# Kernel optimization log

Measured on AMD Instinct MI355X. Metric: run time of the kernel, lower is better.

The kernel has to match this reference:

```python
import jax, jax.numpy as jnp
import numpy as np

NUM_HEADS = 12

def setup_inputs() -> dict:
    key = jax.random.key(0)
    ks = jax.random.split(key, 6)
    B, N, C = 16, 1024, 768
    H, d = NUM_HEADS, C // NUM_HEADS
    return {
        "x": jax.random.normal(ks[0], (B, N, C), dtype=jnp.float32),
        "W_qkv": jax.random.normal(ks[1], (C, 3 * C), dtype=jnp.float32) * 0.02,
        "b_qkv": jax.random.normal(ks[2], (3 * C,), dtype=jnp.float32) * 0.02,
        "zeta": jnp.ones((1, 1, H, 1, d), dtype=jnp.float32),
        "W_proj": jax.random.normal(ks[3], (C, C), dtype=jnp.float32) * 0.02,
        "b_proj": jax.random.normal(ks[4], (C,), dtype=jnp.float32) * 0.02,
        "mask": jnp.zeros((B, N), dtype=bool),
    }

def reference(x, W_qkv, b_qkv, zeta, W_proj, b_proj, mask):
    B, N, C = x.shape
    H = NUM_HEADS
    d = C // H
    scale = d ** -0.5
    # qkv: (B,N,3C) -> (B,N,3,H,d) -> (3,B,H,N,d), gated by zeta (1,1,H,1,d)
    qkv = (x @ W_qkv + b_qkv).reshape(B, N, 3, H, d).transpose(2, 0, 3, 1, 4)
    qkv = qkv * zeta
    q, k, v = qkv[0], qkv[1], qkv[2]
    attn = jnp.einsum("bhnd,bhmd->bhnm", q, k) * scale
    # mask (B,N) over keys -> (B,1,1,N)
    attn = jnp.where(mask[:, None, None, :], -jnp.inf, attn)
    attn = jax.nn.softmax(attn, axis=-1)
    out = jnp.einsum("bhnm,bhmd->bhnd", attn, v)          # (B,H,N,d)
    out = out.transpose(0, 2, 1, 3).reshape(B, N, C)
    return out @ W_proj + b_proj
```

## Files before the change

### kernel.cpp

```cpp
#include <hip/hip_runtime.h>
#include <hip/hip_bf16.h>

typedef unsigned short ushort_t;
typedef __bf16 bf16_t;
typedef bf16_t bf16x8 __attribute__((ext_vector_type(8)));
typedef float floatx4 __attribute__((ext_vector_type(4)));
typedef ushort_t ushortx8 __attribute__((ext_vector_type(8)));

struct alignas(8) us4 { ushort_t x, y, z, w; };

__device__ __forceinline__ ushort_t f2bf(float f) {
  union { float f; unsigned int u; } v; v.f = f;
  unsigned int u = v.u;
  return (ushort_t)((u + 0x7fffu + ((u >> 16) & 1u)) >> 16);
}

__device__ __forceinline__ unsigned int pk_bf16(float a, float b) {
  __hip_bfloat162 h = __float22bfloat162_rn(float2{a, b});
  union { __hip_bfloat162 h; unsigned int u; } v; v.h = h;
  return v.u;
}

__device__ __forceinline__ void async16(const void* g, void* l) {
  __builtin_amdgcn_global_load_lds(
      (const __attribute__((address_space(1))) unsigned int*)g,
      (__attribute__((address_space(3))) unsigned int*)l, 16, 0, 0);
}

#define LOG2E 1.44269504088896340736f


__global__ __launch_bounds__(256) void k_prep(const float* __restrict__ x,
                                              ushort_t* __restrict__ xb,
                                              const float* __restrict__ Wq,
                                              ushort_t* __restrict__ WqT,
                                              const float* __restrict__ Wp,
                                              ushort_t* __restrict__ WpT) {
  __shared__ float tile[32][33];
  const int bid = blockIdx.x, t = threadIdx.x;
  if (bid < 6144) {
    size_t i = ((size_t)bid * 256 + t) * 8;
    float4 a = *(const float4*)(x + i);
    float4 b = *(const float4*)(x + i + 4);
    ushortx8 o;
    o[0] = f2bf(a.x); o[1] = f2bf(a.y); o[2] = f2bf(a.z); o[3] = f2bf(a.w);
    o[4] = f2bf(b.x); o[5] = f2bf(b.y); o[6] = f2bf(b.z); o[7] = f2bf(b.w);
    *(ushortx8*)(xb + i) = o;
    return;
  }
  const float* in; ushort_t* out; int C, c0, r0;
  if (bid < 7872) {
    int b2 = bid - 6144;
    in = Wq; out = WqT; C = 2304;
    c0 = (b2 % 72) * 32; r0 = (b2 / 72) * 32;
  } else {
    int b3 = bid - 7872;
    in = Wp; out = WpT; C = 768;
    c0 = (b3 % 24) * 32; r0 = (b3 / 24) * 32;
  }
  const int tx = t & 31, ty = t >> 5;
#pragma unroll
  for (int i = 0; i < 32; i += 8)
    tile[ty + i][tx] = in[(size_t)(r0 + ty + i) * C + c0 + tx];
  __syncthreads();
#pragma unroll
  for (int i = 0; i < 32; i += 8)
    out[(size_t)(c0 + ty + i) * 768 + r0 + tx] = f2bf(tile[tx][ty + i]);
}


template <bool SWAP>
__device__ __forceinline__ void gemm_pipe3(const ushort_t* __restrict__ A,
                                           const ushort_t* __restrict__ Bt,
                                           int m0, int n0,
                                           ushort_t* sA, ushort_t* sB,
                                           floatx4 acc[4][4]) {
  const int t = threadIdx.x;
  const int lane = t & 63;
  const int lr = lane & 15, qd = lane >> 4;
  const int w = t >> 6;
  const int wr = w >> 1, wc = w & 1;
  const int swz = ((t & 3) ^ ((t >> 3) & 3)) * 8;
  const ushort_t* gA = A + (size_t)(m0 + (t >> 2)) * 768 + swz;
  const ushort_t* gB = Bt + (size_t)(n0 + (t >> 2)) * 768 + swz;
  char* lA = (char*)sA + t * 16;
  char* lB = (char*)sB + t * 16;
  const int rsz = (qd ^ ((lr >> 1) & 3)) * 16;
#define ISSUE(kk, buf)                                    \
  do {                                                    \
    const int k0_ = (kk) * 32, b_ = (buf) * 8192;         \
    async16(gA + k0_, lA + b_);                           \
    async16(gA + k0_ + 64 * 768, lA + b_ + 4096);         \
    async16(gB + k0_, lB + b_);                           \
    async16(gB + k0_ + 64 * 768, lB + b_ + 4096);         \
  } while (0)
  ISSUE(0, 0);
  ISSUE(1, 1);
  asm volatile("s_waitcnt vmcnt(4)" ::: "memory");
  asm volatile("s_barrier" ::: "memory");
#pragma unroll
  for (int k = 0; k < 24; ++k) {
    if (k + 2 < 24) ISSUE(k + 2, (k + 2) % 3);
    const char* cA = (const char*)sA + (k % 3) * 8192;
    const char* cB = (const char*)sB + (k % 3) * 8192;
    bf16x8 af[4], bfr[4];
#pragma unroll
    for (int i = 0; i < 4; ++i)
      af[i] = *(const bf16x8*)(cA + (wr * 64 + i * 16 + lr) * 64 + rsz);
#pragma unroll
    for (int j = 0; j < 4; ++j)
      bfr[j] = *(const bf16x8*)(cB + (wc * 64 + j * 16 + lr) * 64 + rsz);
#pragma unroll
    for (int i = 0; i < 4; ++i)
#pragma unroll
      for (int j = 0; j < 4; ++j) {
        if constexpr (SWAP)
          acc[i][j] = __builtin_amdgcn_mfma_f32_16x16x32_bf16(bfr[j], af[i], acc[i][j], 0, 0, 0);
        else
          acc[i][j] = __builtin_amdgcn_mfma_f32_16x16x32_bf16(af[i], bfr[j], acc[i][j], 0, 0, 0);
      }
    if (k < 22)
      asm volatile("s_waitcnt vmcnt(4)" ::: "memory");
    else if (k == 22)
      asm volatile("s_waitcnt vmcnt(0)" ::: "memory");
    if (k < 23) asm volatile("s_barrier" ::: "memory");
  }
#undef ISSUE
}


__global__ __launch_bounds__(256, 3) void k_qkv(const ushort_t* __restrict__ xb,
                                                const ushort_t* __restrict__ WqT,
                                                const float* __restrict__ bqkv,
                                                const float* __restrict__ zeta,
                                                ushort_t* __restrict__ qb,
                                                ushort_t* __restrict__ kb,
                                                ushort_t* __restrict__ vtb) {
  __shared__ alignas(16) ushort_t sA[3 * 4096];
  __shared__ alignas(16) ushort_t sB[3 * 4096];
  floatx4 acc[4][4] = {};
  const int lin = blockIdx.x;
  const int xcd = lin & 7, idx = lin >> 3;
  const int m0 = (xcd * 16 + (idx & 15)) * 128;
  const int n0 = (idx >> 4) * 128;
  const int tq = n0 / 768;
  const int t = threadIdx.x, lane = t & 63, w = t >> 6;
  const int wr = w >> 1, wc = w & 1, lr = lane & 15, qd = lane >> 4;
  if (tq < 2) {
    gemm_pipe3<true>(xb, WqT, m0, n0, sA, sB, acc);
    ushort_t* dst = (tq == 0) ? qb : kb;
    const float sc = (tq == 0) ? 0.125f * LOG2E : 1.0f;
#pragma unroll
    for (int j = 0; j < 4; ++j) {
      int n = n0 + wc * 64 + j * 16 + qd * 4;
      int nc = n - tq * 768;
      int h = nc >> 6, dim = n & 63;
      float4 b4 = *(const float4*)&bqkv[n];
      float4 z4 = *(const float4*)&zeta[nc];
      float g0 = z4.x * sc, g1 = z4.y * sc, g2 = z4.z * sc, g3 = z4.w * sc;
#pragma unroll
      for (int i = 0; i < 4; ++i) {
        int m = m0 + wr * 64 + i * 16 + lr;
        int b = m >> 10, seq = m & 1023;
        us4 pk;
        pk.x = f2bf((acc[i][j][0] + b4.x) * g0);
        pk.y = f2bf((acc[i][j][1] + b4.y) * g1);
        pk.z = f2bf((acc[i][j][2] + b4.z) * g2);
        pk.w = f2bf((acc[i][j][3] + b4.w) * g3);
        *(us4*)&dst[(((size_t)b * 12 + h) * 1024 + seq) * 64 + dim] = pk;
      }
    }
  } else {
    gemm_pipe3<false>(xb, WqT, m0, n0, sA, sB, acc);
#pragma unroll
    for (int j = 0; j < 4; ++j) {
      int n = n0 + wc * 64 + j * 16 + lr;
      int nc = n - 2 * 768;
      int h = nc >> 6, dim = n & 63;
      float bias = bqkv[n];
      float zv = zeta[nc];
#pragma unroll
      for (int i = 0; i < 4; ++i) {
        int mbase = m0 + wr * 64 + i * 16 + qd * 4;
        int b = mbase >> 10, seq = mbase & 1023;
        us4 pk;
        pk.x = f2bf((acc[i][j][0] + bias) * zv);
        pk.y = f2bf((acc[i][j][1] + bias) * zv);
        pk.z = f2bf((acc[i][j][2] + bias) * zv);
        pk.w = f2bf((acc[i][j][3] + bias) * zv);
        *(us4*)&vtb[(((size_t)b * 12 + h) * 64 + dim) * 1024 + seq] = pk;
      }
    }
  }
}


__global__ __launch_bounds__(256, 3) void k_attn(const ushort_t* __restrict__ qg,
                                                 const ushort_t* __restrict__ kg,
                                                 const ushort_t* __restrict__ vg,
                                                 const unsigned char* __restrict__ mask,
                                                 ushort_t* __restrict__ ob) {
  __shared__ alignas(16) char smem[49664];
  char* sV = smem + 32768;
  float* maskadd = (float*)(smem + 49152);
  const int t = threadIdx.x, lane = t & 63, w = t >> 6;
  const int lr = lane & 15, qd = lane >> 4;
  const int lin = blockIdx.x;
  const int bh = (lin & 7) + 8 * (lin >> 6);
  const int qt = (lin >> 3) & 7;
  const int b = bh / 12, h = bh % 12;
  const int qrow0 = qt * 128 + w * 32;
  const ushort_t* qp = qg + (size_t)bh * 65536;
  const ushort_t* kp = kg + (size_t)bh * 65536;
  const ushort_t* vp = vg + (size_t)bh * 65536;
  const unsigned char* mp = mask + b * 1024;

  bf16x8 qf[2][2];
#pragma unroll
  for (int ns = 0; ns < 2; ++ns)
#pragma unroll
    for (int kk = 0; kk < 2; ++kk)
      qf[ns][kk] = *(const bf16x8*)(qp + (size_t)(qrow0 + ns * 16 + lr) * 64 + kk * 32 + qd * 8);

  floatx4 o[4][2] = {};
  float lst[2] = {0.f, 0.f};
  char* sPw = smem + 16384 + w * 4096;

  for (int kt = 0; kt < 8; ++kt) {
    __syncthreads();
    const ushort_t* kpt = kp + kt * 8192;
#pragma unroll
    for (int it = 0; it < 4; ++it) {
      int p = it * 256 + t;
      int r = p >> 3, cs = (p & 7) ^ (r & 7);
      async16(kpt + r * 64 + cs * 8, smem + p * 16);
    }
    const ushort_t* vpt = vp + kt * 128;
#pragma unroll
    for (int it = 0; it < 4; ++it) {
      int p = it * 256 + t;
      int r = p >> 4, cs = (p & 15) ^ (r & 15);
      async16(vpt + (size_t)r * 1024 + cs * 8, sV + p * 16);
    }
    if (t < 128) maskadd[t] = mp[kt * 128 + t] ? -1e30f : 0.0f;
    asm volatile("s_waitcnt vmcnt(0)" ::: "memory");
    __syncthreads();

#pragma unroll
    for (int hh = 0; hh < 2; ++hh) {
      floatx4 s[4][2] = {};
#pragma unroll
      for (int kk = 0; kk < 2; ++kk) {
#pragma unroll
        for (int ms = 0; ms < 4; ++ms) {
          bf16x8 ak = *(const bf16x8*)(smem + ((hh * 4 + ms) * 16 + lr) * 128 +
                                       ((kk * 4 + qd) ^ (lr & 7)) * 16);
#pragma unroll
          for (int ns = 0; ns < 2; ++ns)
            s[ms][ns] = __builtin_amdgcn_mfma_f32_16x16x32_bf16(ak, qf[ns][kk], s[ms][ns], 0, 0, 0);
        }
      }
#pragma unroll
      for (int ms = 0; ms < 4; ++ms) {
        float4 mk = *(const float4*)&maskadd[(hh * 4 + ms) * 16 + qd * 4];
#pragma unroll
        for (int ns = 0; ns < 2; ++ns) {
          float p0 = __builtin_amdgcn_exp2f(s[ms][ns][0] + mk.x);
          float p1 = __builtin_amdgcn_exp2f(s[ms][ns][1] + mk.y);
          float p2 = __builtin_amdgcn_exp2f(s[ms][ns][2] + mk.z);
          float p3 = __builtin_amdgcn_exp2f(s[ms][ns][3] + mk.w);
          lst[ns] += (p0 + p1) + (p2 + p3);
          uint2 pk;
          pk.x = pk_bf16(p0, p1);
          pk.y = pk_bf16(p2, p3);
          *(uint2*)(sPw + (ns * 16 + lr) * 128 +
                    ((ms * 2 + (qd >> 1)) ^ (lr & 7)) * 16 + (qd & 1) * 8) = pk;
        }
      }
      asm volatile("s_waitcnt lgkmcnt(0)" ::: "memory");
#pragma unroll
      for (int kk = 0; kk < 2; ++kk) {
        bf16x8 pb[2];
#pragma unroll
        for (int ns = 0; ns < 2; ++ns)
          pb[ns] = *(const bf16x8*)(sPw + (ns * 16 + lr) * 128 +
                                    ((kk * 4 + qd) ^ (lr & 7)) * 16);
#pragma unroll
        for (int ds = 0; ds < 4; ++ds) {
          bf16x8 av = *(const bf16x8*)(sV + (ds * 16 + lr) * 256 +
                                       ((hh * 8 + kk * 4 + qd) ^ lr) * 16);
#pragma unroll
          for (int ns = 0; ns < 2; ++ns)
            o[ds][ns] = __builtin_amdgcn_mfma_f32_16x16x32_bf16(av, pb[ns], o[ds][ns], 0, 0, 0);
        }
      }
    }
  }
#pragma unroll
  for (int ns = 0; ns < 2; ++ns) {
    lst[ns] += __shfl_xor(lst[ns], 16);
    lst[ns] += __shfl_xor(lst[ns], 32);
  }
#pragma unroll
  for (int ns = 0; ns < 2; ++ns) {
    float rl = 1.0f / lst[ns];
    size_t row = (size_t)(b * 1024 + qrow0 + ns * 16 + lr) * 768 + h * 64;
#pragma unroll
    for (int ds = 0; ds < 4; ++ds) {
      uint2 ov;
      ov.x = pk_bf16(o[ds][ns][0] * rl, o[ds][ns][1] * rl);
      ov.y = pk_bf16(o[ds][ns][2] * rl, o[ds][ns][3] * rl);
      *(uint2*)&ob[row + ds * 16 + qd * 4] = ov;
    }
  }
}


__global__ __launch_bounds__(256, 3) void k_proj(const ushort_t* __restrict__ ob,
                                                 const ushort_t* __restrict__ WpT,
                                                 const float* __restrict__ bproj,
                                                 float* __restrict__ out) {
  __shared__ alignas(16) ushort_t sA[3 * 4096];
  __shared__ alignas(16) ushort_t sB[3 * 4096];
  floatx4 acc[4][4] = {};
  const int lin = blockIdx.x;
  const int xcd = lin & 7, idx = lin >> 3;
  const int m0 = (xcd * 16 + (idx & 15)) * 128;
  const int n0 = (idx >> 4) * 128;
  gemm_pipe3<true>(ob, WpT, m0, n0, sA, sB, acc);
  const int t = threadIdx.x, lane = t & 63, w = t >> 6;
  const int wr = w >> 1, wc = w & 1, lr = lane & 15, qd = lane >> 4;
#pragma unroll
  for (int j = 0; j < 4; ++j) {
    int n = n0 + wc * 64 + j * 16 + qd * 4;
    float4 b4 = *(const float4*)&bproj[n];
#pragma unroll
    for (int i = 0; i < 4; ++i) {
      int m = m0 + wr * 64 + i * 16 + lr;
      float4 o;
      o.x = acc[i][j][0] + b4.x;
      o.y = acc[i][j][1] + b4.y;
      o.z = acc[i][j][2] + b4.z;
      o.w = acc[i][j][3] + b4.w;
      *(float4*)&out[(size_t)m * 768 + n] = o;
    }
  }
}


extern "C" void kernel_launch(void* const* d_in, const int* in_sizes, int n_in,
                              void* d_out, int out_size, void* d_ws, size_t ws_size,
                              hipStream_t stream) {
  const float* x = (const float*)d_in[0];
  const float* bqkv = (const float*)d_in[2];
  const float* zeta = (const float*)d_in[3];
  const float* bproj = (const float*)d_in[5];
  const unsigned char* mask = (const unsigned char*)d_in[6];
  float* out = (float*)d_out;
  char* ws = (char*)d_ws;
  ushort_t* xb  = (ushort_t*)(ws);
  ushort_t* WqT = (ushort_t*)(ws + 25165824);
  ushort_t* WpT = (ushort_t*)(ws + 28704768);
  ushort_t* qb  = (ushort_t*)(ws + 29884416);
  ushort_t* kb  = (ushort_t*)(ws + 55050240);
  ushort_t* vtb = (ushort_t*)(ws + 80216064);
  ushort_t* ob  = xb;

  k_prep<<<dim3(8448), dim3(256), 0, stream>>>(x, xb, (const float*)d_in[1], WqT,
                                               (const float*)d_in[4], WpT);
  k_qkv<<<dim3(2304), dim3(256), 0, stream>>>(xb, WqT, bqkv, zeta, qb, kb, vtb);
  k_attn<<<dim3(1536), dim3(256), 0, stream>>>(qb, kb, vtb, mask, ob);
  k_proj<<<dim3(768), dim3(256), 0, stream>>>(ob, WpT, bproj, out);
}
```

Measured before the change: 299.9 us.

## Enlarge GEMM tiles to 256x128 with double-buffered LDS pipeline

The QKV and projection GEMMs now use 256x128 output tiles per block (8x4 MFMA accumulators per wave) instead of 128x128. The LDS pipeline drops from three stages to two to fit the larger A tile, and occupancy bounds fall from 3 to 2 blocks per CU. This raises arithmetic intensity and halves the block count, at the cost of higher register pressure, less prefetch depth, and fewer blocks (384 for proj), which may underfill the 256 CUs.

Result: no change. 303.1 us (+1.1%).

```diff
diff --git a/kernel.cpp b/kernel.cpp
--- a/kernel.cpp
+++ b/kernel.cpp
@@ -70,11 +70,11 @@
 
 
 template <bool SWAP>
-__device__ __forceinline__ void gemm_pipe3(const ushort_t* __restrict__ A,
+__device__ __forceinline__ void gemm_pipe2(const ushort_t* __restrict__ A,
                                            const ushort_t* __restrict__ Bt,
                                            int m0, int n0,
                                            ushort_t* sA, ushort_t* sB,
-                                           floatx4 acc[4][4]) {
+                                           floatx4 acc[8][4]) {
   const int t = threadIdx.x;
   const int lane = t & 63;
   const int lr = lane & 15, qd = lane >> 4;
@@ -88,30 +88,32 @@
   const int rsz = (qd ^ ((lr >> 1) & 3)) * 16;
 #define ISSUE(kk, buf)                                    \
   do {                                                    \
-    const int k0_ = (kk) * 32, b_ = (buf) * 8192;         \
-    async16(gA + k0_, lA + b_);                           \
-    async16(gA + k0_ + 64 * 768, lA + b_ + 4096);         \
-    async16(gB + k0_, lB + b_);                           \
-    async16(gB + k0_ + 64 * 768, lB + b_ + 4096);         \
+    const int k0_ = (kk) * 32;                            \
+    const int ba_ = (buf) * 16384, bb_ = (buf) * 8192;    \
+    async16(gA + k0_, lA + ba_);                          \
+    async16(gA + k0_ + 64 * 768, lA + ba_ + 4096);        \
+    async16(gA + k0_ + 128 * 768, lA + ba_ + 8192);       \
+    async16(gA + k0_ + 192 * 768, lA + ba_ + 12288);      \
+    async16(gB + k0_, lB + bb_);                          \
+    async16(gB + k0_ + 64 * 768, lB + bb_ + 4096);        \
   } while (0)
   ISSUE(0, 0);
-  ISSUE(1, 1);
-  asm volatile("s_waitcnt vmcnt(4)" ::: "memory");
+  asm volatile("s_waitcnt vmcnt(0)" ::: "memory");
   asm volatile("s_barrier" ::: "memory");
 #pragma unroll
   for (int k = 0; k < 24; ++k) {
-    if (k + 2 < 24) ISSUE(k + 2, (k + 2) % 3);
-    const char* cA = (const char*)sA + (k % 3) * 8192;
-    const char* cB = (const char*)sB + (k % 3) * 8192;
-    bf16x8 af[4], bfr[4];
-#pragma unroll
-    for (int i = 0; i < 4; ++i)
-      af[i] = *(const bf16x8*)(cA + (wr * 64 + i * 16 + lr) * 64 + rsz);
+    if (k + 1 < 24) ISSUE(k + 1, (k + 1) & 1);
+    const char* cA = (const char*)sA + (k & 1) * 16384;
+    const char* cB = (const char*)sB + (k & 1) * 8192;
+    bf16x8 af[8], bfr[4];
+#pragma unroll
+    for (int i = 0; i < 8; ++i)
+      af[i] = *(const bf16x8*)(cA + (wr * 128 + i * 16 + lr) * 64 + rsz);
 #pragma unroll
     for (int j = 0; j < 4; ++j)
       bfr[j] = *(const bf16x8*)(cB + (wc * 64 + j * 16 + lr) * 64 + rsz);
 #pragma unroll
-    for (int i = 0; i < 4; ++i)
+    for (int i = 0; i < 8; ++i)
 #pragma unroll
       for (int j = 0; j < 4; ++j) {
         if constexpr (SWAP)
@@ -119,9 +121,7 @@
         else
           acc[i][j] = __builtin_amdgcn_mfma_f32_16x16x32_bf16(af[i], bfr[j], acc[i][j], 0, 0, 0);
       }
-    if (k < 22)
-      asm volatile("s_waitcnt vmcnt(4)" ::: "memory");
-    else if (k == 22)
+    if (k + 1 < 24)
       asm volatile("s_waitcnt vmcnt(0)" ::: "memory");
     if (k < 23) asm volatile("s_barrier" ::: "memory");
   }
@@ -129,25 +129,25 @@
 }
 
 
-__global__ __launch_bounds__(256, 3) void k_qkv(const ushort_t* __restrict__ xb,
+__global__ __launch_bounds__(256, 2) void k_qkv(const ushort_t* __restrict__ xb,
                                                 const ushort_t* __restrict__ WqT,
                                                 const float* __restrict__ bqkv,
                                                 const float* __restrict__ zeta,
                                                 ushort_t* __restrict__ qb,
                                                 ushort_t* __restrict__ kb,
                                                 ushort_t* __restrict__ vtb) {
-  __shared__ alignas(16) ushort_t sA[3 * 4096];
-  __shared__ alignas(16) ushort_t sB[3 * 4096];
-  floatx4 acc[4][4] = {};
+  __shared__ alignas(16) ushort_t sA[2 * 8192];
+  __shared__ alignas(16) ushort_t sB[2 * 4096];
+  floatx4 acc[8][4] = {};
   const int lin = blockIdx.x;
   const int xcd = lin & 7, idx = lin >> 3;
-  const int m0 = (xcd * 16 + (idx & 15)) * 128;
-  const int n0 = (idx >> 4) * 128;
+  const int m0 = (xcd * 8 + (idx & 7)) * 256;
+  const int n0 = (idx >> 3) * 128;
   const int tq = n0 / 768;
   const int t = threadIdx.x, lane = t & 63, w = t >> 6;
   const int wr = w >> 1, wc = w & 1, lr = lane & 15, qd = lane >> 4;
   if (tq < 2) {
-    gemm_pipe3<true>(xb, WqT, m0, n0, sA, sB, acc);
+    gemm_pipe2<true>(xb, WqT, m0, n0, sA, sB, acc);
     ushort_t* dst = (tq == 0) ? qb : kb;
     const float sc = (tq == 0) ? 0.125f * LOG2E : 1.0f;
 #pragma unroll
@@ -159,8 +159,8 @@
       float4 z4 = *(const float4*)&zeta[nc];
       float g0 = z4.x * sc, g1 = z4.y * sc, g2 = z4.z * sc, g3 = z4.w * sc;
 #pragma unroll
-      for (int i = 0; i < 4; ++i) {
-        int m = m0 + wr * 64 + i * 16 + lr;
+      for (int i = 0; i < 8; ++i) {
+        int m = m0 + wr * 128 + i * 16 + lr;
         int b = m >> 10, seq = m & 1023;
         us4 pk;
         pk.x = f2bf((acc[i][j][0] + b4.x) * g0);
@@ -171,7 +171,7 @@
       }
     }
   } else {
-    gemm_pipe3<false>(xb, WqT, m0, n0, sA, sB, acc);
+    gemm_pipe2<false>(xb, WqT, m0, n0, sA, sB, acc);
 #pragma unroll
     for (int j = 0; j < 4; ++j) {
       int n = n0 + wc * 64 + j * 16 + lr;
@@ -180,8 +180,8 @@
       float bias = bqkv[n];
       float zv = zeta[nc];
 #pragma unroll
-      for (int i = 0; i < 4; ++i) {
-        int mbase = m0 + wr * 64 + i * 16 + qd * 4;
+      for (int i = 0; i < 8; ++i) {
+        int mbase = m0 + wr * 128 + i * 16 + qd * 4;
         int b = mbase >> 10, seq = mbase & 1023;
         us4 pk;
         pk.x = f2bf((acc[i][j][0] + bias) * zv);
@@ -316,18 +316,18 @@
 }
 
 
-__global__ __launch_bounds__(256, 3) void k_proj(const ushort_t* __restrict__ ob,
+__global__ __launch_bounds__(256, 2) void k_proj(const ushort_t* __restrict__ ob,
                                                  const ushort_t* __restrict__ WpT,
                                                  const float* __restrict__ bproj,
                                                  float* __restrict__ out) {
-  __shared__ alignas(16) ushort_t sA[3 * 4096];
-  __shared__ alignas(16) ushort_t sB[3 * 4096];
-  floatx4 acc[4][4] = {};
+  __shared__ alignas(16) ushort_t sA[2 * 8192];
+  __shared__ alignas(16) ushort_t sB[2 * 4096];
+  floatx4 acc[8][4] = {};
   const int lin = blockIdx.x;
   const int xcd = lin & 7, idx = lin >> 3;
-  const int m0 = (xcd * 16 + (idx & 15)) * 128;
-  const int n0 = (idx >> 4) * 128;
-  gemm_pipe3<true>(ob, WpT, m0, n0, sA, sB, acc);
+  const int m0 = (xcd * 8 + (idx & 7)) * 256;
+  const int n0 = (idx >> 3) * 128;
+  gemm_pipe2<true>(ob, WpT, m0, n0, sA, sB, acc);
   const int t = threadIdx.x, lane = t & 63, w = t >> 6;
   const int wr = w >> 1, wc = w & 1, lr = lane & 15, qd = lane >> 4;
 #pragma unroll
@@ -335,8 +335,8 @@
     int n = n0 + wc * 64 + j * 16 + qd * 4;
     float4 b4 = *(const float4*)&bproj[n];
 #pragma unroll
-    for (int i = 0; i < 4; ++i) {
-      int m = m0 + wr * 64 + i * 16 + lr;
+    for (int i = 0; i < 8; ++i) {
+      int m = m0 + wr * 128 + i * 16 + lr;
       float4 o;
       o.x = acc[i][j][0] + b4.x;
       o.y = acc[i][j][1] + b4.y;
@@ -368,7 +368,7 @@
 
   k_prep<<<dim3(8448), dim3(256), 0, stream>>>(x, xb, (const float*)d_in[1], WqT,
                                                (const float*)d_in[4], WpT);
-  k_qkv<<<dim3(2304), dim3(256), 0, stream>>>(xb, WqT, bqkv, zeta, qb, kb, vtb);
+  k_qkv<<<dim3(1152), dim3(256), 0, stream>>>(xb, WqT, bqkv, zeta, qb, kb, vtb);
   k_attn<<<dim3(1536), dim3(256), 0, stream>>>(qb, kb, vtb, mask, ob);
-  k_proj<<<dim3(768), dim3(256), 0, stream>>>(ob, WpT, bproj, out);
-}
+  k_proj<<<dim3(384), dim3(256), 0, stream>>>(ob, WpT, bproj, out);
+}
```

## Double-buffer K/V tiles in attention with async prefetch and wave priority

Applied to the files above, without the earlier changes.

The attention loop now uses 64-key tiles with two LDS stages. The next tile's K and V are loaded asynchronously while the current tile is computed, and partial vmcnt waits plus raw s_barrier replace the full sync-then-wait at each step. The key mask is converted to additive floats once up front instead of per tile, and s_setprio raises priority around the MFMA phases. This is meant to hide global load latency behind compute, at the cost of more LDS per block and finer, more fragile synchronisation.

Result: faster. 290.2 us (-3.2%).

```diff
diff --git a/kernel.cpp b/kernel.cpp
--- a/kernel.cpp
+++ b/kernel.cpp
@@ -200,8 +200,7 @@
                                                  const ushort_t* __restrict__ vg,
                                                  const unsigned char* __restrict__ mask,
                                                  ushort_t* __restrict__ ob) {
-  __shared__ alignas(16) char smem[49664];
-  char* sV = smem + 32768;
+  __shared__ alignas(16) char smem[53248];
   float* maskadd = (float*)(smem + 49152);
   const int t = threadIdx.x, lane = t & 63, w = t >> 6;
   const int lr = lane & 15, qd = lane >> 4;
@@ -224,78 +223,122 @@
 
   floatx4 o[4][2] = {};
   float lst[2] = {0.f, 0.f};
-  char* sPw = smem + 16384 + w * 4096;
-
-  for (int kt = 0; kt < 8; ++kt) {
-    __syncthreads();
-    const ushort_t* kpt = kp + kt * 8192;
-#pragma unroll
-    for (int it = 0; it < 4; ++it) {
-      int p = it * 256 + t;
-      int r = p >> 3, cs = (p & 7) ^ (r & 7);
-      async16(kpt + r * 64 + cs * 8, smem + p * 16);
-    }
-    const ushort_t* vpt = vp + kt * 128;
-#pragma unroll
-    for (int it = 0; it < 4; ++it) {
-      int p = it * 256 + t;
-      int r = p >> 4, cs = (p & 15) ^ (r & 15);
-      async16(vpt + (size_t)r * 1024 + cs * 8, sV + p * 16);
-    }
-    if (t < 128) maskadd[t] = mp[kt * 128 + t] ? -1e30f : 0.0f;
-    asm volatile("s_waitcnt vmcnt(0)" ::: "memory");
-    __syncthreads();
-
-#pragma unroll
-    for (int hh = 0; hh < 2; ++hh) {
-      floatx4 s[4][2] = {};
-#pragma unroll
-      for (int kk = 0; kk < 2; ++kk) {
-#pragma unroll
-        for (int ms = 0; ms < 4; ++ms) {
-          bf16x8 ak = *(const bf16x8*)(smem + ((hh * 4 + ms) * 16 + lr) * 128 +
-                                       ((kk * 4 + qd) ^ (lr & 7)) * 16);
-#pragma unroll
-          for (int ns = 0; ns < 2; ++ns)
-            s[ms][ns] = __builtin_amdgcn_mfma_f32_16x16x32_bf16(ak, qf[ns][kk], s[ms][ns], 0, 0, 0);
-        }
-      }
+  char* sPw = smem + 32768 + w * 4096;
+
+  {
+    uchar4 mv = *(const uchar4*)(mp + t * 4);
+    float4 f;
+    f.x = mv.x ? -1e30f : 0.0f;
+    f.y = mv.y ? -1e30f : 0.0f;
+    f.z = mv.z ? -1e30f : 0.0f;
+    f.w = mv.w ? -1e30f : 0.0f;
+    *(float4*)&maskadd[t * 4] = f;
+  }
+
+#define STAGE_K(kt_, st_)                                                 \
+  do {                                                                    \
+    const ushort_t* kpt_ = kp + (kt_) * 4096;                             \
+    _Pragma("unroll")                                                     \
+    for (int it = 0; it < 2; ++it) {                                      \
+      int p = it * 256 + t;                                               \
+      int r = p >> 3, cs = (p & 7) ^ (r & 7);                             \
+      async16(kpt_ + r * 64 + cs * 8, smem + (st_) * 16384 + p * 16);     \
+    }                                                                     \
+  } while (0)
+#define STAGE_V(kt_, st_)                                                 \
+  do {                                                                    \
+    const ushort_t* vpt_ = vp + (kt_) * 64;                               \
+    _Pragma("unroll")                                                     \
+    for (int it = 0; it < 2; ++it) {                                      \
+      int p = it * 256 + t;                                               \
+      int r = p >> 3, cs = (p & 7) ^ (r & 7);                             \
+      async16(vpt_ + (size_t)r * 1024 + cs * 8,                           \
+              smem + (st_) * 16384 + 8192 + p * 16);                      \
+    }                                                                     \
+  } while (0)
+
+  STAGE_K(0, 0);
+  STAGE_V(0, 0);
+  __syncthreads();
+
+#pragma unroll 2
+  for (int kt = 0; kt < 16; ++kt) {
+    const int st = kt & 1;
+    if (kt + 1 < 16) {
+      STAGE_K(kt + 1, st ^ 1);
+      STAGE_V(kt + 1, st ^ 1);
+    }
+    const char* sK = smem + st * 16384;
+    const char* sV = smem + st * 16384 + 8192;
+
+    floatx4 s[4][2] = {};
+    __builtin_amdgcn_s_setprio(1);
+#pragma unroll
+    for (int kk = 0; kk < 2; ++kk) {
 #pragma unroll
       for (int ms = 0; ms < 4; ++ms) {
-        float4 mk = *(const float4*)&maskadd[(hh * 4 + ms) * 16 + qd * 4];
-#pragma unroll
-        for (int ns = 0; ns < 2; ++ns) {
-          float p0 = __builtin_amdgcn_exp2f(s[ms][ns][0] + mk.x);
-          float p1 = __builtin_amdgcn_exp2f(s[ms][ns][1] + mk.y);
-          float p2 = __builtin_amdgcn_exp2f(s[ms][ns][2] + mk.z);
-          float p3 = __builtin_amdgcn_exp2f(s[ms][ns][3] + mk.w);
-          lst[ns] += (p0 + p1) + (p2 + p3);
-          uint2 pk;
-          pk.x = pk_bf16(p0, p1);
-          pk.y = pk_bf16(p2, p3);
-          *(uint2*)(sPw + (ns * 16 + lr) * 128 +
-                    ((ms * 2 + (qd >> 1)) ^ (lr & 7)) * 16 + (qd & 1) * 8) = pk;
-        }
-      }
-      asm volatile("s_waitcnt lgkmcnt(0)" ::: "memory");
-#pragma unroll
-      for (int kk = 0; kk < 2; ++kk) {
-        bf16x8 pb[2];
+        bf16x8 ak = *(const bf16x8*)(sK + (ms * 16 + lr) * 128 +
+                                     ((kk * 4 + qd) ^ (lr & 7)) * 16);
 #pragma unroll
         for (int ns = 0; ns < 2; ++ns)
-          pb[ns] = *(const bf16x8*)(sPw + (ns * 16 + lr) * 128 +
-                                    ((kk * 4 + qd) ^ (lr & 7)) * 16);
-#pragma unroll
-        for (int ds = 0; ds < 4; ++ds) {
-          bf16x8 av = *(const bf16x8*)(sV + (ds * 16 + lr) * 256 +
-                                       ((hh * 8 + kk * 4 + qd) ^ lr) * 16);
-#pragma unroll
-          for (int ns = 0; ns < 2; ++ns)
-            o[ds][ns] = __builtin_amdgcn_mfma_f32_16x16x32_bf16(av, pb[ns], o[ds][ns], 0, 0, 0);
-        }
-      }
-    }
-  }
+          s[ms][ns] = __builtin_amdgcn_mfma_f32_16x16x32_bf16(ak, qf[ns][kk], s[ms][ns], 0, 0, 0);
+      }
+    }
+    __builtin_amdgcn_s_setprio(0);
+
+#pragma unroll
+    for (int ms = 0; ms < 4; ++ms) {
+      float4 mk = *(const float4*)&maskadd[kt * 64 + ms * 16 + qd * 4];
+#pragma unroll
+      for (int ns = 0; ns < 2; ++ns) {
+        float p0 = __builtin_amdgcn_exp2f(s[ms][ns][0] + mk.x);
+        float p1 = __builtin_amdgcn_exp2f(s[ms][ns][1] + mk.y);
+        float p2 = __builtin_amdgcn_exp2f(s[ms][ns][2] + mk.z);
+        float p3 = __builtin_amdgcn_exp2f(s[ms][ns][3] + mk.w);
+        lst[ns] += (p0 + p1) + (p2 + p3);
+        uint2 pk;
+        pk.x = pk_bf16(p0, p1);
+        pk.y = pk_bf16(p2, p3);
+        *(uint2*)(sPw + (ns * 16 + lr) * 128 +
+                  ((ms * 2 + (qd >> 1)) ^ (lr & 7)) * 16 + (qd & 1) * 8) = pk;
+      }
+    }
+    asm volatile("s_waitcnt lgkmcnt(0)" ::: "memory");
+    __builtin_amdgcn_sched_barrier(0);
+
+    if (kt + 1 < 16)
+      asm volatile("s_waitcnt vmcnt(4)" ::: "memory");
+    else
+      asm volatile("s_waitcnt vmcnt(0)" ::: "memory");
+    asm volatile("s_barrier" ::: "memory");
+
+    __builtin_amdgcn_s_setprio(1);
+#pragma unroll
+    for (int kk = 0; kk < 2; ++kk) {
+      bf16x8 pb[2];
+#pragma unroll
+      for (int ns = 0; ns < 2; ++ns)
+        pb[ns] = *(const bf16x8*)(sPw + (ns * 16 + lr) * 128 +
+                                  ((kk * 4 + qd) ^ (lr & 7)) * 16);
+#pragma unroll
+      for (int ds = 0; ds < 4; ++ds) {
+        bf16x8 av = *(const bf16x8*)(sV + (ds * 16 + lr) * 128 +
+                                     ((kk * 4 + qd) ^ (lr & 7)) * 16);
+#pragma unroll
+        for (int ns = 0; ns < 2; ++ns)
+          o[ds][ns] = __builtin_amdgcn_mfma_f32_16x16x32_bf16(av, pb[ns], o[ds][ns], 0, 0, 0);
+      }
+    }
+    __builtin_amdgcn_s_setprio(0);
+
+    if (kt + 1 < 16) {
+      asm volatile("s_waitcnt vmcnt(2)" ::: "memory");
+      asm volatile("s_barrier" ::: "memory");
+    }
+  }
+#undef STAGE_K
+#undef STAGE_V
+
 #pragma unroll
   for (int ns = 0; ns < 2; ++ns) {
     lst[ns] += __shfl_xor(lst[ns], 16);
```
